# Kernel optimization log

Measured on AMD Instinct MI355X. Metric: run time of the kernel, lower is better.

The kernel has to match this reference:

```python
import jax, jax.numpy as jnp
import numpy as np

N_NODES = 50000
N_EDGES = 800000
N_GRAPHS = 512
D_IN, D_HID, D_EMB = 64, 128, 128


def _lin_params(key, d_in, d_out):
    kw, kb = jax.random.split(key)
    scale = 1.0 / np.sqrt(d_in)
    W = jax.random.uniform(kw, (d_in, d_out), minval=-scale, maxval=scale, dtype=jnp.float32)
    b = jax.random.uniform(kb, (d_out,), minval=-scale, maxval=scale, dtype=jnp.float32)
    return W, b


def setup_inputs() -> dict:
    key = jax.random.key(0)
    ks = jax.random.split(key, 12)
    x = jax.random.normal(ks[0], (N_NODES, D_IN), dtype=jnp.float32)
    edge_index = jax.random.randint(ks[1], (2, N_EDGES), 0, N_NODES, dtype=jnp.int64)
    batch = jnp.sort(jax.random.randint(ks[2], (N_NODES,), 0, N_GRAPHS, dtype=jnp.int64))
    Wq1, bq1 = _lin_params(ks[3], D_IN, D_HID)
    Wk1, bk1 = _lin_params(ks[4], D_IN, D_HID)
    Wv1, bv1 = _lin_params(ks[5], D_IN, D_HID)
    Ws1, bs1 = _lin_params(ks[6], D_IN, D_HID)
    Wq2, bq2 = _lin_params(ks[7], D_HID, D_EMB)
    Wk2, bk2 = _lin_params(ks[8], D_HID, D_EMB)
    Wv2, bv2 = _lin_params(ks[9], D_HID, D_EMB)
    Ws2, bs2 = _lin_params(ks[10], D_HID, D_EMB)
    return {
        'x': x, 'edge_index': edge_index, 'batch': batch,
        'Wq1': Wq1, 'bq1': bq1, 'Wk1': Wk1, 'bk1': bk1, 'Wv1': Wv1, 'bv1': bv1, 'Ws1': Ws1, 'bs1': bs1,
        'Wq2': Wq2, 'bq2': bq2, 'Wk2': Wk2, 'bk2': bk2, 'Wv2': Wv2, 'bv2': bv2, 'Ws2': Ws2, 'bs2': bs2,
    }


def _transformer_conv(x, src, dst, Wq, bq, Wk, bk, Wv, bv, Ws, bs):
    # PyG TransformerConv, heads=1, concat=True, root_weight=True, no edge_attr.
    d = Wq.shape[1]
    q = x @ Wq + bq          # [N, d]
    k = x @ Wk + bk
    v = x @ Wv + bv
    # per-edge attention score (gather at src/dst)
    score = jnp.sum(q[dst] * k[src], axis=-1) / jnp.sqrt(jnp.float32(d))  # [E]
    # segment softmax over destination neighborhoods
    m = jax.ops.segment_max(score, dst, num_segments=N_NODES)
    e = jnp.exp(score - m[dst])
    s = jax.ops.segment_sum(e, dst, num_segments=N_NODES)
    alpha = e / (s[dst] + 1e-16)  # [E]
    out = jax.ops.segment_sum(alpha[:, None] * v[src], dst, num_segments=N_NODES)  # [N, d]
    return out + (x @ Ws + bs)  # skip connection


def reference(x, edge_index, batch,
              Wq1, bq1, Wk1, bk1, Wv1, bv1, Ws1, bs1,
              Wq2, bq2, Wk2, bk2, Wv2, bv2, Ws2, bs2):
    src, dst = edge_index[0], edge_index[1]
    h = _transformer_conv(x, src, dst, Wq1, bq1, Wk1, bk1, Wv1, bv1, Ws1, bs1)
    h = jax.nn.relu(h)
    h = _transformer_conv(h, src, dst, Wq2, bq2, Wk2, bk2, Wv2, bv2, Ws2, bs2)
    # global mean pool over batch index
    sums = jax.ops.segment_sum(h, batch, num_segments=N_GRAPHS)
    counts = jax.ops.segment_sum(jnp.ones((h.shape[0],), dtype=h.dtype), batch, num_segments=N_GRAPHS)
    return sums / jnp.maximum(counts, 1.0)[:, None]
```

## Files before the change

### kernel.cpp

```cpp
#include <hip/hip_runtime.h>
#include <hip/hip_fp8.h>
#include <math.h>


constexpr int D1 = 64;
constexpr int DH = 128;
constexpr int SCHUNK = 1024;
constexpr float QSCALE = 0.08838834764831845f;

typedef __attribute__((ext_vector_type(8))) short short8v;
typedef __attribute__((ext_vector_type(4))) float f32x4;

__device__ inline unsigned short bf16r(float f) {
  unsigned u = __float_as_uint(f);
  return (unsigned short)((u + 0x7fffu + ((u >> 16) & 1u)) >> 16);
}

__device__ inline unsigned pack_bf16_2(float a, float b) {
  return (unsigned)bf16r(a) | ((unsigned)bf16r(b) << 16);
}

__device__ inline float bf16f(unsigned short u) {
  return __uint_as_float(((unsigned)u) << 16);
}

__device__ inline float fp8f(unsigned b) {
  __hip_fp8_e4m3 h;
  h.__x = (unsigned char)b;
  return (float)h;
}

__device__ inline unsigned char fp8e(float f) {
  __hip_fp8_e4m3 h(f);
  return h.__x;
}


__global__ __launch_bounds__(256) void hist_prep(
    const int* __restrict__ dst, int* __restrict__ deg, int* __restrict__ rank,
    int E, int nbHist,
    const float* w0, const float* w1, const float* w2, const float* w3,
    const float* w4, const float* w5, const float* w6, const float* w7,
    unsigned short* t0, unsigned short* t1, unsigned short* t2,
    unsigned short* t3, unsigned short* t4, unsigned short* t5,
    unsigned short* t6, unsigned short* t7,
    const float4* __restrict__ x, uint2* __restrict__ xb, int n4) {
  int b = blockIdx.x;
  int tid = threadIdx.x;
  if (b < nbHist) {
    int i = b * 256 + tid;
    if (i < (E >> 2)) {
      int4 d4 = ((const int4*)dst)[i];
      int4 r4;
      r4.x = atomicAdd(&deg[d4.x], 1);
      r4.y = atomicAdd(&deg[d4.y], 1);
      r4.z = atomicAdd(&deg[d4.z], 1);
      r4.w = atomicAdd(&deg[d4.w], 1);
      ((int4*)rank)[i] = r4;
    }
    if (b == 0 && tid == 0) {
      for (int e = E & ~3; e < E; ++e) rank[e] = atomicAdd(&deg[dst[e]], 1);
    }
    return;
  }
  int g = b - nbHist;
  if (g < 512) {
    int m = g >> 6, bx = g & 63;
    const float* W;
    unsigned short* T;
    switch (m) {
      case 0: W = w0; T = t0; break;
      case 1: W = w1; T = t1; break;
      case 2: W = w2; T = t2; break;
      case 3: W = w3; T = t3; break;
      case 4: W = w4; T = t4; break;
      case 5: W = w5; T = t5; break;
      case 6: W = w6; T = t6; break;
      default: W = w7; T = t7; break;
    }
    int din = (m < 4) ? 64 : 128;
    int total = din * 128;
    int i = bx * 256 + tid;
    if (i < total) {
      int r = i >> 7, c = i & 127;
      T[c * din + r] = bf16r(W[i]);
    }
    return;
  }
  int bx = g - 512;
  for (int i = bx * 256 + tid; i < n4; i += 256 * 256) {
    float4 v = x[i];
    uint2 o;
    o.x = pack_bf16_2(v.x, v.y);
    o.y = pack_bf16_2(v.z, v.w);
    xb[i] = o;
  }
}


__global__ void scan_chunks(const int* __restrict__ deg, int* __restrict__ incl,
                            int* __restrict__ sums, int N) {
  __shared__ int lds[256];
  int b = blockIdx.x, tid = threadIdx.x;
  int base = b * SCHUNK + tid * 4;
  int e0 = (base + 0 < N) ? deg[base + 0] : 0;
  int e1 = (base + 1 < N) ? deg[base + 1] : 0;
  int e2 = (base + 2 < N) ? deg[base + 2] : 0;
  int e3 = (base + 3 < N) ? deg[base + 3] : 0;
  int t0 = e0, t1 = t0 + e1, t2 = t1 + e2, t3 = t2 + e3;
  lds[tid] = t3;
  __syncthreads();
  for (int off = 1; off < 256; off <<= 1) {
    int v = (tid >= off) ? lds[tid - off] : 0;
    __syncthreads();
    lds[tid] += v;
    __syncthreads();
  }
  int excl = (tid > 0) ? lds[tid - 1] : 0;
  if (base + 0 < N) incl[base + 0] = t0 + excl;
  if (base + 1 < N) incl[base + 1] = t1 + excl;
  if (base + 2 < N) incl[base + 2] = t2 + excl;
  if (base + 3 < N) incl[base + 3] = t3 + excl;
  if (tid == 255) sums[b] = lds[255];
}

__global__ void finalize_rowptr(const int* __restrict__ incl, const int* __restrict__ sums,
                                int* __restrict__ rowptr, int N) {
  int n = blockIdx.x * blockDim.x + threadIdx.x;
  if (n < N) {
    int ch = n / SCHUNK;
    int off = 0;
    for (int i = 0; i < ch; ++i) off += sums[i];
    rowptr[n + 1] = incl[n] + off;
  }
  if (n == 0) rowptr[0] = 0;
}


template <int DIN>
__device__ __forceinline__ void gemm4_tile(
    int bx, int y, int tid,
    const unsigned short* __restrict__ xb, int N,
    const unsigned short* __restrict__ Wt0, const float* __restrict__ B0,
    const unsigned short* __restrict__ Wt1, const float* __restrict__ B1,
    const unsigned short* __restrict__ Wt2, const float* __restrict__ B2,
    const unsigned short* __restrict__ Wt3, const float* __restrict__ B3,
    unsigned short* __restrict__ Qb, unsigned char* __restrict__ KV,
    float* __restrict__ Os) {
  constexpr int DS = DIN + 8;
  __shared__ __align__(16) unsigned short As[128 * DS];
  __shared__ __align__(16) unsigned short Bs[128 * DS];
  const unsigned short* Wt;
  const float* Bias;
  switch (y) {
    case 0: Wt = Wt0; Bias = B0; break;
    case 1: Wt = Wt1; Bias = B1; break;
    case 2: Wt = Wt2; Bias = B2; break;
    default: Wt = Wt3; Bias = B3; break;
  }
  int n0 = bx * 128;

  constexpr int CPR = DIN / 8;
  constexpr int ACH = 128 * CPR;
#pragma unroll
  for (int c = tid; c < ACH; c += 512) {
    int row = c / CPR, c8 = c - row * CPR;
    int n = n0 + row;
    uint4 val = {0u, 0u, 0u, 0u};
    if (n < N) val = *(const uint4*)&xb[(size_t)n * DIN + c8 * 8];
    *(uint4*)&As[row * DS + c8 * 8] = val;
  }
#pragma unroll
  for (int c = tid; c < ACH; c += 512) {
    int row = c / CPR, c8 = c - row * CPR;
    uint4 val = *(const uint4*)&Wt[(size_t)row * DIN + c8 * 8];
    *(uint4*)&Bs[row * DS + c8 * 8] = val;
  }
  __syncthreads();

  int w = tid >> 6, lane = tid & 63, lr = lane & 15, lg = lane >> 4;
  int wr = w >> 2;
  int wc = w & 3;
  constexpr int KS = DIN / 32;

  short8v a[4][KS];
#pragma unroll
  for (int af = 0; af < 4; ++af)
#pragma unroll
    for (int ks = 0; ks < KS; ++ks)
      a[af][ks] = *(const short8v*)&As[(wr * 64 + af * 16 + lr) * DS + ks * 32 + lg * 8];

  f32x4 acc[4][2];
#pragma unroll
  for (int af = 0; af < 4; ++af)
#pragma unroll
    for (int nf = 0; nf < 2; ++nf) acc[af][nf] = (f32x4){0.f, 0.f, 0.f, 0.f};

#pragma unroll
  for (int ks = 0; ks < KS; ++ks) {
#pragma unroll
    for (int nf = 0; nf < 2; ++nf) {
      short8v b = *(const short8v*)&Bs[(wc * 32 + nf * 16 + lr) * DS + ks * 32 + lg * 8];
#pragma unroll
      for (int af = 0; af < 4; ++af)
        acc[af][nf] = __builtin_amdgcn_mfma_f32_16x16x32_bf16(a[af][ks], b, acc[af][nf], 0, 0, 0);
    }
  }

#pragma unroll
  for (int af = 0; af < 4; ++af) {
    int rbase = n0 + wr * 64 + af * 16 + lg * 4;
#pragma unroll
    for (int nf = 0; nf < 2; ++nf) {
      int col = wc * 32 + nf * 16 + lr;
      float bias = Bias[col];
      if (y == 0) {
#pragma unroll
        for (int r = 0; r < 4; ++r) {
          int n = rbase + r;
          if (n < N) Qb[(size_t)n * 128 + col] = bf16r((acc[af][nf][r] + bias) * QSCALE);
        }
      } else if (y == 1) {
#pragma unroll
        for (int r = 0; r < 4; ++r) {
          int n = rbase + r;
          if (n < N) KV[(size_t)n * 384 + col] = fp8e(acc[af][nf][r] + bias);
        }
      } else if (y == 2) {
#pragma unroll
        for (int r = 0; r < 4; ++r) {
          int n = rbase + r;
          if (n < N)
            *(unsigned short*)&KV[(size_t)n * 384 + 128 + col * 2] =
                bf16r(acc[af][nf][r] + bias);
        }
      } else {
#pragma unroll
        for (int r = 0; r < 4; ++r) {
          int n = rbase + r;
          if (n < N) Os[(size_t)n * 128 + col] = acc[af][nf][r] + bias;
        }
      }
    }
  }
}


template <int DIN>
__global__ __launch_bounds__(512) void fill_gemm1(
    const int* __restrict__ src, const int* __restrict__ dst,
    const int* __restrict__ rank, const int* __restrict__ rowptr,
    int* __restrict__ csr_src, int E, int epb4,
    const unsigned short* __restrict__ xb, int N,
    const unsigned short* __restrict__ Wt0, const float* __restrict__ B0,
    const unsigned short* __restrict__ Wt1, const float* __restrict__ B1,
    const unsigned short* __restrict__ Wt2, const float* __restrict__ B2,
    const unsigned short* __restrict__ Wt3, const float* __restrict__ B3,
    unsigned short* __restrict__ Qb, unsigned char* __restrict__ KV,
    float* __restrict__ Os) {
  int b = blockIdx.x;
  int b5 = b / 5, r5 = b - b5 * 5;
  if (r5 == 0) {
    int e4 = E >> 2;
    int end = min((b5 + 1) * epb4, e4);
    for (int i = b5 * epb4 + threadIdx.x; i < end; i += 512) {
      int4 d4 = ((const int4*)dst)[i];
      int4 r4 = ((const int4*)rank)[i];
      int4 s4 = ((const int4*)src)[i];
      csr_src[rowptr[d4.x] + r4.x] = s4.x;
      csr_src[rowptr[d4.y] + r4.y] = s4.y;
      csr_src[rowptr[d4.z] + r4.z] = s4.z;
      csr_src[rowptr[d4.w] + r4.w] = s4.w;
    }
    if (b5 == 0 && threadIdx.x == 0) {
      for (int e = E & ~3; e < E; ++e) csr_src[rowptr[dst[e]] + rank[e]] = src[e];
    }
    return;
  }
  int g = b5 * 4 + r5 - 1;
  gemm4_tile<DIN>(g >> 2, g & 3, threadIdx.x, xb, N, Wt0, B0, Wt1, B1,
                  Wt2, B2, Wt3, B3, Qb, KV, Os);
}

template <int DIN>
__global__ __launch_bounds__(512) void gemm4(
    const unsigned short* __restrict__ xb, int N,
    const unsigned short* __restrict__ Wt0, const float* __restrict__ B0,
    const unsigned short* __restrict__ Wt1, const float* __restrict__ B1,
    const unsigned short* __restrict__ Wt2, const float* __restrict__ B2,
    const unsigned short* __restrict__ Wt3, const float* __restrict__ B3,
    unsigned short* __restrict__ Qb, unsigned char* __restrict__ KV,
    float* __restrict__ Os) {
  gemm4_tile<DIN>(blockIdx.x, blockIdx.y, threadIdx.x, xb, N, Wt0, B0, Wt1, B1,
                  Wt2, B2, Wt3, B3, Qb, KV, Os);
}


template <bool RELU, bool OUTBF16>
__global__ __launch_bounds__(256) void edge_agg2(
    const unsigned short* __restrict__ qb, const unsigned char* __restrict__ kv,
    const int* __restrict__ rowptr, const int* __restrict__ csr_src,
    const float* skip, void* outp, int N) {
  int tid = threadIdx.x;
  int lane = tid & 63;
  int wv = tid >> 6;
  int n = blockIdx.x * 4 + wv;
  if (n >= N) return;
  int g = lane >> 5;
  int l = lane & 31;
  uint2 qp = *(const uint2*)&qb[(size_t)n * 128 + 4 * l];
  float qx = __uint_as_float(qp.x << 16);
  float qy = __uint_as_float(qp.x & 0xffff0000u);
  float qz = __uint_as_float(qp.y << 16);
  float qw = __uint_as_float(qp.y & 0xffff0000u);
  int beg = rowptr[n];
  int deg = rowptr[n + 1] - beg;
  float m = -INFINITY, lsum = 0.f;
  float a0 = 0.f, a1 = 0.f, a2 = 0.f, a3 = 0.f;
  int cnt = (deg - g + 1) >> 1;
  const int* cp = csr_src + beg + g;
  unsigned kw0 = 0, kw1 = 0, kw2 = 0;
  uint2 vw0 = {0, 0}, vw1 = {0, 0}, vw2 = {0, 0};
  if (cnt >= 1) {
    size_t r = (size_t)cp[0] * 384;
    kw0 = *(const unsigned*)(kv + r + 4 * l);
    vw0 = *(const uint2*)(kv + r + 128 + 8 * l);
  }
  if (cnt >= 2) {
    size_t r = (size_t)cp[2] * 384;
    kw1 = *(const unsigned*)(kv + r + 4 * l);
    vw1 = *(const uint2*)(kv + r + 128 + 8 * l);
  }
  if (cnt >= 3) {
    size_t r = (size_t)cp[4] * 384;
    kw2 = *(const unsigned*)(kv + r + 4 * l);
    vw2 = *(const uint2*)(kv + r + 128 + 8 * l);
  }
  for (int it = 0; it < cnt; ++it) {
    unsigned kc = kw0;
    uint2 vc = vw0;
    kw0 = kw1; kw1 = kw2;
    vw0 = vw1; vw1 = vw2;
    if (it + 3 < cnt) {
      size_t r = (size_t)cp[2 * (it + 3)] * 384;
      kw2 = *(const unsigned*)(kv + r + 4 * l);
      vw2 = *(const uint2*)(kv + r + 128 + 8 * l);
    }
    float k0 = fp8f(kc & 0xffu);
    float k1 = fp8f((kc >> 8) & 0xffu);
    float k2 = fp8f((kc >> 16) & 0xffu);
    float k3 = fp8f(kc >> 24);
    float d = qx * k0 + qy * k1 + qz * k2 + qw * k3;
#pragma unroll
    for (int off = 1; off < 32; off <<= 1) d += __shfl_xor(d, off);
    float v0 = __uint_as_float(vc.x << 16);
    float v1 = __uint_as_float(vc.x & 0xffff0000u);
    float v2 = __uint_as_float(vc.y << 16);
    float v3 = __uint_as_float(vc.y & 0xffff0000u);
    if (d > m + 8.f) {
      float cf = __expf(m - d);
      lsum = lsum * cf + 1.f;
      a0 = a0 * cf + v0;
      a1 = a1 * cf + v1;
      a2 = a2 * cf + v2;
      a3 = a3 * cf + v3;
      m = d;
    } else {
      float ef = __expf(d - m);
      lsum += ef;
      a0 += ef * v0;
      a1 += ef * v1;
      a2 += ef * v2;
      a3 += ef * v3;
    }
  }
  float m2 = __shfl_xor(m, 32);
  float L2 = __shfl_xor(lsum, 32);
  float b0 = __shfl_xor(a0, 32);
  float b1 = __shfl_xor(a1, 32);
  float b2 = __shfl_xor(a2, 32);
  float b3 = __shfl_xor(a3, 32);
  if (lane < 32) {
    float ox0 = 0.f, ox1 = 0.f, ox2 = 0.f, ox3 = 0.f;
    if (deg > 0) {
      float M = fmaxf(m, m2);
      float c1 = __expf(m - M);
      float c2 = __expf(m2 - M);
      float rl = 1.f / (lsum * c1 + L2 * c2 + 1e-16f);
      ox0 = (a0 * c1 + b0 * c2) * rl;
      ox1 = (a1 * c1 + b1 * c2) * rl;
      ox2 = (a2 * c1 + b2 * c2) * rl;
      ox3 = (a3 * c1 + b3 * c2) * rl;
    }
    const float* sp = skip + (size_t)n * 128 + 4 * l;
    float4 o = *(const float4*)sp;
    o.x += ox0; o.y += ox1; o.z += ox2; o.w += ox3;
    if (RELU) {
      o.x = fmaxf(o.x, 0.f);
      o.y = fmaxf(o.y, 0.f);
      o.z = fmaxf(o.z, 0.f);
      o.w = fmaxf(o.w, 0.f);
    }
    if (OUTBF16) {
      unsigned short* ob = (unsigned short*)outp + (size_t)n * 128 + 4 * l;
      uint2 pk;
      pk.x = pack_bf16_2(o.x, o.y);
      pk.y = pack_bf16_2(o.z, o.w);
      *(uint2*)ob = pk;
    } else {
      float* of = (float*)outp + (size_t)n * 128 + 4 * l;
      *(float4*)of = o;
    }
  }
}


__global__ __launch_bounds__(128) void pool_kernel(const unsigned short* __restrict__ h,
                                                   const int* __restrict__ batch,
                                                   float* __restrict__ out, int N) {
  int g = blockIdx.x;
  int lo = 0, hi = N;
  while (lo < hi) { int mid = (lo + hi) >> 1; if (batch[mid] < g) lo = mid + 1; else hi = mid; }
  int s0 = lo;
  hi = N;
  while (lo < hi) { int mid = (lo + hi) >> 1; if (batch[mid] <= g) lo = mid + 1; else hi = mid; }
  int s1 = lo;
  int j = threadIdx.x;
  float acc = 0.f;
  for (int n = s0; n < s1; ++n) acc += bf16f(h[(size_t)n * 128 + j]);
  out[(size_t)g * 128 + j] = acc / fmaxf((float)(s1 - s0), 1.f);
}


extern "C" void kernel_launch(void* const* d_in, const int* in_sizes, int n_in,
                              void* d_out, int out_size, void* d_ws, size_t ws_size,
                              hipStream_t stream) {
  const float* x = (const float*)d_in[0];
  const int* ei = (const int*)d_in[1];
  const int* batch = (const int*)d_in[2];
  const float* Wq1 = (const float*)d_in[3];
  const float* bq1 = (const float*)d_in[4];
  const float* Wk1 = (const float*)d_in[5];
  const float* bk1 = (const float*)d_in[6];
  const float* Wv1 = (const float*)d_in[7];
  const float* bv1 = (const float*)d_in[8];
  const float* Ws1 = (const float*)d_in[9];
  const float* bs1 = (const float*)d_in[10];
  const float* Wq2 = (const float*)d_in[11];
  const float* bq2 = (const float*)d_in[12];
  const float* Wk2 = (const float*)d_in[13];
  const float* bk2 = (const float*)d_in[14];
  const float* Wv2 = (const float*)d_in[15];
  const float* bv2 = (const float*)d_in[16];
  const float* Ws2 = (const float*)d_in[17];
  const float* bs2 = (const float*)d_in[18];

  int N = in_sizes[0] / D1;
  int E = in_sizes[1] / 2;
  int NG = out_size / DH;
  const int* src = ei;
  const int* dst = ei + E;

  char* ws = (char*)d_ws;
  unsigned short* qb = (unsigned short*)ws;  ws += (size_t)N * DH * 2;
  unsigned char* kvb = (unsigned char*)ws;   ws += (size_t)N * 384;
  ws = (char*)(((size_t)ws + 255) & ~(size_t)255);
  float* s = (float*)ws;             ws += (size_t)N * DH * 4;
  unsigned short* h1b = (unsigned short*)ws; ws += (size_t)N * DH * 2;
  unsigned short* xb = (unsigned short*)ws;  ws += (size_t)N * D1 * 2;
  unsigned short* wt[8];
  for (int m = 0; m < 8; ++m) {
    int din = (m < 4) ? 64 : 128;
    wt[m] = (unsigned short*)ws;
    ws += (size_t)128 * din * 2;
  }
  ws = (char*)(((size_t)ws + 255) & ~(size_t)255);
  int* rowptr = (int*)ws; ws += (size_t)(N + 1) * 4;
  ws = (char*)(((size_t)ws + 255) & ~(size_t)255);
  int* deg = (int*)ws;  ws += (size_t)N * 4;
  int* incl = (int*)ws; ws += (size_t)N * 4;
  int* sums = (int*)ws; ws += 1024;
  int* rank = (int*)ws; ws += (size_t)E * 4;
  int* csr = (int*)ws;  ws += (size_t)E * 4;

  int nch = (N + SCHUNK - 1) / SCHUNK;
  int nbHist = ((E >> 2) + 255) / 256;
  int nb = (N + 127) / 128;
  int epb4 = ((E >> 2) + nb - 1) / nb;

  hipMemsetAsync(deg, 0, (size_t)N * 4, stream);

  hist_prep<<<nbHist + 768, 256, 0, stream>>>(
      dst, deg, rank, E, nbHist, Wq1, Wk1, Wv1, Ws1, Wq2, Wk2, Wv2, Ws2,
      wt[0], wt[1], wt[2], wt[3], wt[4], wt[5], wt[6], wt[7],
      (const float4*)x, (uint2*)xb, N * D1 / 4);
  scan_chunks<<<nch, 256, 0, stream>>>(deg, incl, sums, N);
  finalize_rowptr<<<(N + 255) / 256, 256, 0, stream>>>(incl, sums, rowptr, N);
  fill_gemm1<D1><<<nb * 5, 512, 0, stream>>>(
      src, dst, rank, rowptr, csr, E, epb4, xb, N,
      wt[0], bq1, wt[1], bk1, wt[2], bv1, wt[3], bs1, qb, kvb, s);
  edge_agg2<true, true><<<(N + 3) / 4, 256, 0, stream>>>(
      qb, kvb, rowptr, csr, s, h1b, N);
  gemm4<DH><<<dim3(nb, 4), 512, 0, stream>>>(h1b, N, wt[4], bq2, wt[5], bk2,
                                             wt[6], bv2, wt[7], bs2, qb, kvb, s);
  edge_agg2<false, true><<<(N + 3) / 4, 256, 0, stream>>>(
      qb, kvb, rowptr, csr, s, h1b, N);
  pool_kernel<<<NG, 128, 0, stream>>>(h1b, batch, (float*)d_out, N);
}
```

Before: 275.5 us.

## Split each wavefront into four 16-lane edge groups with hardware fp8 decode

```diff
diff --git a/kernel.cpp b/kernel.cpp
--- a/kernel.cpp
+++ b/kernel.cpp
@@ -10,6 +10,11 @@
 
 typedef __attribute__((ext_vector_type(8))) short short8v;
 typedef __attribute__((ext_vector_type(4))) float f32x4;
+typedef __attribute__((ext_vector_type(2))) float f32x2;
+
+#if __has_builtin(__builtin_amdgcn_cvt_pk_f32_fp8)
+#define HW_FP8_DEC 1
+#endif
 
 __device__ inline unsigned short bf16r(float f) {
   unsigned u = __float_as_uint(f);
@@ -24,16 +29,20 @@
   return __uint_as_float(((unsigned)u) << 16);
 }
 
-__device__ inline float fp8f(unsigned b) {
-  __hip_fp8_e4m3 h;
-  h.__x = (unsigned char)b;
-  return (float)h;
-}
-
 __device__ inline unsigned char fp8e(float f) {
   __hip_fp8_e4m3 h(f);
   return h.__x;
 }
+
+#ifndef HW_FP8_DEC
+__device__ inline float fp8f_sw(unsigned b) {
+  unsigned e = (b >> 3) & 15u, mm = b & 7u;
+  float v;
+  if (e == 0) v = (float)mm * 0.001953125f;
+  else v = __uint_as_float(((e + 119u) << 23) | (mm << 20));
+  return (b & 0x80u) ? -v : v;
+}
+#endif
 
 
 __global__ __launch_bounds__(256) void hist_prep(
@@ -296,121 +305,125 @@
 }
 
 
-template <bool RELU, bool OUTBF16>
-__global__ __launch_bounds__(256) void edge_agg2(
+template <bool RELU>
+__global__ __launch_bounds__(256) void edge_agg4(
     const unsigned short* __restrict__ qb, const unsigned char* __restrict__ kv,
     const int* __restrict__ rowptr, const int* __restrict__ csr_src,
-    const float* skip, void* outp, int N) {
+    const float* skip, unsigned short* __restrict__ outp, int N) {
   int tid = threadIdx.x;
   int lane = tid & 63;
   int wv = tid >> 6;
   int n = blockIdx.x * 4 + wv;
   if (n >= N) return;
-  int g = lane >> 5;
-  int l = lane & 31;
-  uint2 qp = *(const uint2*)&qb[(size_t)n * 128 + 4 * l];
-  float qx = __uint_as_float(qp.x << 16);
-  float qy = __uint_as_float(qp.x & 0xffff0000u);
-  float qz = __uint_as_float(qp.y << 16);
-  float qw = __uint_as_float(qp.y & 0xffff0000u);
+  int g4 = lane >> 4;
+  int sl = lane & 15;
+  uint4 qp = *(const uint4*)&qb[(size_t)n * 128 + 8 * sl];
+  float q0 = bf16f((unsigned short)(qp.x & 0xffff)), q1 = bf16f((unsigned short)(qp.x >> 16));
+  float q2 = bf16f((unsigned short)(qp.y & 0xffff)), q3 = bf16f((unsigned short)(qp.y >> 16));
+  float q4 = bf16f((unsigned short)(qp.z & 0xffff)), q5 = bf16f((unsigned short)(qp.z >> 16));
+  float q6 = bf16f((unsigned short)(qp.w & 0xffff)), q7 = bf16f((unsigned short)(qp.w >> 16));
   int beg = rowptr[n];
   int deg = rowptr[n + 1] - beg;
-  float m = -INFINITY, lsum = 0.f;
-  float a0 = 0.f, a1 = 0.f, a2 = 0.f, a3 = 0.f;
-  int cnt = (deg - g + 1) >> 1;
-  const int* cp = csr_src + beg + g;
-  unsigned kw0 = 0, kw1 = 0, kw2 = 0;
-  uint2 vw0 = {0, 0}, vw1 = {0, 0}, vw2 = {0, 0};
+  float m = -1e30f, lsum = 0.f;
+  float acc[8];
+#pragma unroll
+  for (int j = 0; j < 8; ++j) acc[j] = 0.f;
+  int cnt = (deg - g4 + 3) >> 2;
+  if (cnt < 0) cnt = 0;
+  const int* cp = csr_src + beg + g4;
+  unsigned ko = 8u * sl, vo = 128u + 16u * sl;
+  uint2 k0 = {0, 0}, k1 = {0, 0};
+  uint4 v0 = {0, 0, 0, 0}, v1 = {0, 0, 0, 0};
   if (cnt >= 1) {
-    size_t r = (size_t)cp[0] * 384;
-    kw0 = *(const unsigned*)(kv + r + 4 * l);
-    vw0 = *(const uint2*)(kv + r + 128 + 8 * l);
+    unsigned r = (unsigned)cp[0] * 384u;
+    k0 = *(const uint2*)(kv + r + ko);
+    v0 = *(const uint4*)(kv + r + vo);
   }
   if (cnt >= 2) {
-    size_t r = (size_t)cp[2] * 384;
-    kw1 = *(const unsigned*)(kv + r + 4 * l);
-    vw1 = *(const uint2*)(kv + r + 128 + 8 * l);
-  }
-  if (cnt >= 3) {
-    size_t r = (size_t)cp[4] * 384;
-    kw2 = *(const unsigned*)(kv + r + 4 * l);
-    vw2 = *(const uint2*)(kv + r + 128 + 8 * l);
+    unsigned r = (unsigned)cp[4] * 384u;
+    k1 = *(const uint2*)(kv + r + ko);
+    v1 = *(const uint4*)(kv + r + vo);
   }
   for (int it = 0; it < cnt; ++it) {
-    unsigned kc = kw0;
-    uint2 vc = vw0;
-    kw0 = kw1; kw1 = kw2;
-    vw0 = vw1; vw1 = vw2;
-    if (it + 3 < cnt) {
-      size_t r = (size_t)cp[2 * (it + 3)] * 384;
-      kw2 = *(const unsigned*)(kv + r + 4 * l);
-      vw2 = *(const uint2*)(kv + r + 128 + 8 * l);
-    }
-    float k0 = fp8f(kc & 0xffu);
-    float k1 = fp8f((kc >> 8) & 0xffu);
-    float k2 = fp8f((kc >> 16) & 0xffu);
-    float k3 = fp8f(kc >> 24);
-    float d = qx * k0 + qy * k1 + qz * k2 + qw * k3;
-#pragma unroll
-    for (int off = 1; off < 32; off <<= 1) d += __shfl_xor(d, off);
-    float v0 = __uint_as_float(vc.x << 16);
-    float v1 = __uint_as_float(vc.x & 0xffff0000u);
-    float v2 = __uint_as_float(vc.y << 16);
-    float v3 = __uint_as_float(vc.y & 0xffff0000u);
+    uint2 kc = k0;
+    uint4 vc = v0;
+    k0 = k1;
+    v0 = v1;
+    if (it + 2 < cnt) {
+      unsigned r = (unsigned)cp[4 * (it + 2)] * 384u;
+      k1 = *(const uint2*)(kv + r + ko);
+      v1 = *(const uint4*)(kv + r + vo);
+    }
+#ifdef HW_FP8_DEC
+    f32x2 p01 = __builtin_amdgcn_cvt_pk_f32_fp8((int)kc.x, false);
+    f32x2 p23 = __builtin_amdgcn_cvt_pk_f32_fp8((int)kc.x, true);
+    f32x2 p45 = __builtin_amdgcn_cvt_pk_f32_fp8((int)kc.y, false);
+    f32x2 p67 = __builtin_amdgcn_cvt_pk_f32_fp8((int)kc.y, true);
+    float d = q0 * p01[0] + q1 * p01[1] + q2 * p23[0] + q3 * p23[1] +
+              q4 * p45[0] + q5 * p45[1] + q6 * p67[0] + q7 * p67[1];
+#else
+    float d = q0 * fp8f_sw(kc.x & 0xffu) + q1 * fp8f_sw((kc.x >> 8) & 0xffu) +
+              q2 * fp8f_sw((kc.x >> 16) & 0xffu) + q3 * fp8f_sw(kc.x >> 24) +
+              q4 * fp8f_sw(kc.y & 0xffu) + q5 * fp8f_sw((kc.y >> 8) & 0xffu) +
+              q6 * fp8f_sw((kc.y >> 16) & 0xffu) + q7 * fp8f_sw(kc.y >> 24);
+#endif
+#pragma unroll
+    for (int off = 1; off < 16; off <<= 1) d += __shfl_xor(d, off);
+    float w0 = bf16f((unsigned short)(vc.x & 0xffff)), w1 = bf16f((unsigned short)(vc.x >> 16));
+    float w2 = bf16f((unsigned short)(vc.y & 0xffff)), w3 = bf16f((unsigned short)(vc.y >> 16));
+    float w4 = bf16f((unsigned short)(vc.z & 0xffff)), w5 = bf16f((unsigned short)(vc.z >> 16));
+    float w6 = bf16f((unsigned short)(vc.w & 0xffff)), w7 = bf16f((unsigned short)(vc.w >> 16));
     if (d > m + 8.f) {
       float cf = __expf(m - d);
       lsum = lsum * cf + 1.f;
-      a0 = a0 * cf + v0;
-      a1 = a1 * cf + v1;
-      a2 = a2 * cf + v2;
-      a3 = a3 * cf + v3;
+      acc[0] = acc[0] * cf + w0; acc[1] = acc[1] * cf + w1;
+      acc[2] = acc[2] * cf + w2; acc[3] = acc[3] * cf + w3;
+      acc[4] = acc[4] * cf + w4; acc[5] = acc[5] * cf + w5;
+      acc[6] = acc[6] * cf + w6; acc[7] = acc[7] * cf + w7;
       m = d;
     } else {
       float ef = __expf(d - m);
       lsum += ef;
-      a0 += ef * v0;
-      a1 += ef * v1;
-      a2 += ef * v2;
-      a3 += ef * v3;
-    }
-  }
-  float m2 = __shfl_xor(m, 32);
-  float L2 = __shfl_xor(lsum, 32);
-  float b0 = __shfl_xor(a0, 32);
-  float b1 = __shfl_xor(a1, 32);
-  float b2 = __shfl_xor(a2, 32);
-  float b3 = __shfl_xor(a3, 32);
-  if (lane < 32) {
-    float ox0 = 0.f, ox1 = 0.f, ox2 = 0.f, ox3 = 0.f;
-    if (deg > 0) {
-      float M = fmaxf(m, m2);
-      float c1 = __expf(m - M);
-      float c2 = __expf(m2 - M);
-      float rl = 1.f / (lsum * c1 + L2 * c2 + 1e-16f);
-      ox0 = (a0 * c1 + b0 * c2) * rl;
-      ox1 = (a1 * c1 + b1 * c2) * rl;
-      ox2 = (a2 * c1 + b2 * c2) * rl;
-      ox3 = (a3 * c1 + b3 * c2) * rl;
-    }
-    const float* sp = skip + (size_t)n * 128 + 4 * l;
-    float4 o = *(const float4*)sp;
-    o.x += ox0; o.y += ox1; o.z += ox2; o.w += ox3;
+      acc[0] += ef * w0; acc[1] += ef * w1;
+      acc[2] += ef * w2; acc[3] += ef * w3;
+      acc[4] += ef * w4; acc[5] += ef * w5;
+      acc[6] += ef * w6; acc[7] += ef * w7;
+    }
+  }
+#pragma unroll
+  for (int ofs = 16; ofs <= 32; ofs <<= 1) {
+    float mo = __shfl_xor(m, ofs);
+    float lo = __shfl_xor(lsum, ofs);
+    float ao[8];
+#pragma unroll
+    for (int j = 0; j < 8; ++j) ao[j] = __shfl_xor(acc[j], ofs);
+    float M = fmaxf(m, mo);
+    float c1 = __expf(m - M);
+    float c2 = __expf(mo - M);
+    lsum = lsum * c1 + lo * c2;
+#pragma unroll
+    for (int j = 0; j < 8; ++j) acc[j] = acc[j] * c1 + ao[j] * c2;
+    m = M;
+  }
+  if (lane < 16) {
+    float rl = (deg > 0) ? 1.f / (lsum + 1e-16f) : 0.f;
+    const float* sp = skip + (size_t)n * 128 + 8 * sl;
+    float4 s0 = ((const float4*)sp)[0];
+    float4 s1 = ((const float4*)sp)[1];
+    float o0 = s0.x + acc[0] * rl, o1 = s0.y + acc[1] * rl;
+    float o2 = s0.z + acc[2] * rl, o3 = s0.w + acc[3] * rl;
+    float o4 = s1.x + acc[4] * rl, o5 = s1.y + acc[5] * rl;
+    float o6 = s1.z + acc[6] * rl, o7 = s1.w + acc[7] * rl;
     if (RELU) {
-      o.x = fmaxf(o.x, 0.f);
-      o.y = fmaxf(o.y, 0.f);
-      o.z = fmaxf(o.z, 0.f);
-      o.w = fmaxf(o.w, 0.f);
-    }
-    if (OUTBF16) {
-      unsigned short* ob = (unsigned short*)outp + (size_t)n * 128 + 4 * l;
-      uint2 pk;
-      pk.x = pack_bf16_2(o.x, o.y);
-      pk.y = pack_bf16_2(o.z, o.w);
-      *(uint2*)ob = pk;
-    } else {
-      float* of = (float*)outp + (size_t)n * 128 + 4 * l;
-      *(float4*)of = o;
-    }
+      o0 = fmaxf(o0, 0.f); o1 = fmaxf(o1, 0.f); o2 = fmaxf(o2, 0.f); o3 = fmaxf(o3, 0.f);
+      o4 = fmaxf(o4, 0.f); o5 = fmaxf(o5, 0.f); o6 = fmaxf(o6, 0.f); o7 = fmaxf(o7, 0.f);
+    }
+    uint4 pk;
+    pk.x = pack_bf16_2(o0, o1);
+    pk.y = pack_bf16_2(o2, o3);
+    pk.z = pack_bf16_2(o4, o5);
+    pk.w = pack_bf16_2(o6, o7);
+    *(uint4*)&outp[(size_t)n * 128 + 8 * sl] = pk;
   }
 }
 
@@ -499,11 +512,11 @@
   fill_gemm1<D1><<<nb * 5, 512, 0, stream>>>(
       src, dst, rank, rowptr, csr, E, epb4, xb, N,
       wt[0], bq1, wt[1], bk1, wt[2], bv1, wt[3], bs1, qb, kvb, s);
-  edge_agg2<true, true><<<(N + 3) / 4, 256, 0, stream>>>(
+  edge_agg4<true><<<(N + 3) / 4, 256, 0, stream>>>(
       qb, kvb, rowptr, csr, s, h1b, N);
   gemm4<DH><<<dim3(nb, 4), 512, 0, stream>>>(h1b, N, wt[4], bq2, wt[5], bk2,
                                              wt[6], bv2, wt[7], bs2, qb, kvb, s);
-  edge_agg2<false, true><<<(N + 3) / 4, 256, 0, stream>>>(
+  edge_agg4<false><<<(N + 3) / 4, 256, 0, stream>>>(
       qb, kvb, rowptr, csr, s, h1b, N);
   pool_kernel<<<NG, 128, 0, stream>>>(h1b, batch, (float*)d_out, N);
 }
```

New measurement: 258.6 us. 6.2% less time.
